# Optimization experiments

Measured on AMD Instinct MI355X. Metric: run time of the kernel, lower is better.

Reference implementation:

```python
import jax, jax.numpy as jnp
import numpy as np

N = 50000
E = 800000
IN_CH = 256
HID = 64
HEADS = 8
OUT_CH = 16
NEG_SLOPE = 0.2


def _glorot(key, shape):
    fan_in, fan_out = shape[0], shape[-1]
    lim = float(np.sqrt(6.0 / (fan_in + fan_out)))
    return jax.random.uniform(key, shape, jnp.float32, -lim, lim)


def setup_inputs() -> dict:
    key = jax.random.key(0)
    ks = jax.random.split(key, 12)
    x = jax.random.normal(ks[0], (N, IN_CH), jnp.float32)
    edge_index = jax.random.randint(ks[1], (2, E), 0, N, jnp.int64)
    # layer 1: GATConv(256 -> 64, heads=8)
    W1 = _glorot(ks[2], (IN_CH, HEADS * HID))
    a_src1 = _glorot(ks[3], (HEADS, HID))
    a_dst1 = _glorot(ks[4], (HEADS, HID))
    b1 = jnp.zeros((HEADS * HID,), jnp.float32)
    # layer 2: GATConv(512 -> 16, heads=1, concat=False)
    W2 = _glorot(ks[5], (HEADS * HID, OUT_CH))
    a_src2 = _glorot(ks[6], (1, OUT_CH))
    a_dst2 = _glorot(ks[7], (1, OUT_CH))
    b2 = jnp.zeros((OUT_CH,), jnp.float32)
    return {"x": x, "edge_index": edge_index, "W1": W1, "a_src1": a_src1,
            "a_dst1": a_dst1, "b1": b1, "W2": W2, "a_src2": a_src2,
            "a_dst2": a_dst2, "b2": b2}


def _gat_conv(x, src, dst, W, a_src, a_dst, bias, heads, out_ch, concat):
    n = x.shape[0]
    h = (x @ W).reshape(n, heads, out_ch)            # [N,H,C]
    alpha_s = jnp.einsum('nhc,hc->nh', h, a_src)      # [N,H]
    alpha_d = jnp.einsum('nhc,hc->nh', h, a_dst)
    e = alpha_s[src] + alpha_d[dst]                   # [E,H]
    e = jnp.where(e > 0, e, NEG_SLOPE * e)            # leaky_relu
    # segment softmax over incoming edges of each dst node
    e_max = jax.ops.segment_max(e, dst, num_segments=n)
    e_max = jnp.where(jnp.isfinite(e_max), e_max, 0.0)
    p = jnp.exp(e - e_max[dst])                       # [E,H]
    denom = jax.ops.segment_sum(p, dst, num_segments=n)
    alpha = p / (denom[dst] + 1e-16)                  # [E,H]
    msg = h[src] * alpha[:, :, None]                  # [E,H,C]
    out = jax.ops.segment_sum(msg, dst, num_segments=n)  # [N,H,C]
    if concat:
        out = out.reshape(n, heads * out_ch)
    else:
        out = out.mean(axis=1)
    return out + bias


def reference(x, edge_index, W1, a_src1, a_dst1, b1, W2, a_src2, a_dst2, b2):
    n = x.shape[0]
    loops = jnp.arange(n, dtype=edge_index.dtype)
    ei = jnp.concatenate([edge_index, jnp.stack([loops, loops])], axis=1)
    src, dst = ei[0], ei[1]
    h = _gat_conv(x, src, dst, W1, a_src1, a_dst1, b1, HEADS, HID, True)
    h = jax.nn.elu(h)
    out = _gat_conv(h, src, dst, W2, a_src2, a_dst2, b2, 1, OUT_CH, False)
    return jax.nn.log_softmax(out, axis=-1)
```

## Files before the change

kernel.cpp:

```cpp
#include <hip/hip_runtime.h>
#include <math.h>

#define IN_CH 256
#define HID 64
#define HEADS 8
#define F1 512
#define OUT_CH 16
#define NEG 0.2f

typedef __attribute__((ext_vector_type(8))) short bf16x8;
typedef __attribute__((ext_vector_type(4))) float f32x4;
typedef __attribute__((ext_vector_type(2))) float f32x2;

__device__ __forceinline__ unsigned short f2bf(float f) {
  unsigned int u = __builtin_bit_cast(unsigned int, f);
  u += 0x7FFFu + ((u >> 16) & 1u);
  return (unsigned short)(u >> 16);
}
__device__ __forceinline__ void gld_lds16(const void* g, void* l) {
  __builtin_amdgcn_global_load_lds(
      (const __attribute__((address_space(1))) unsigned int*)g,
      (__attribute__((address_space(3))) unsigned int*)l, 16, 0, 0);
}


__global__ void prep_kernel(const int* __restrict__ ei, int E, int N,
                            int* counts,
                            const float* __restrict__ W1, unsigned short* __restrict__ W1R,
                            const float* __restrict__ W2, unsigned short* __restrict__ W2T) {
  int idx = blockIdx.x * blockDim.x + threadIdx.x;
  int ET = E + N;
  if (idx < ET) {
    int dst = (idx < E) ? ei[E + idx] : (idx - E);
    atomicAdd(&counts[dst], 1);
  }
  if (idx < F1 * IN_CH) {
    int n = idx >> 8, k = idx & 255;
    int r = (((k >> 5) * 4 + ((k >> 3) & 3)) * 512 + n) * 8 + (k & 7);
    W1R[r] = f2bf(W1[k * F1 + n]);
  }
  if (idx < OUT_CH * F1) {
    int n = idx >> 9, k = idx & 511;
    W2T[idx] = f2bf(W2[k * OUT_CH + n]);
  }
}

__global__ __launch_bounds__(1024) void scan1_kernel(const int* __restrict__ counts,
                                                     int* __restrict__ offsets,
                                                     int* __restrict__ bsum, int n) {
  __shared__ int lds[1024];
  int t = threadIdx.x;
  int i = blockIdx.x * 1024 + t;
  int v = (i < n) ? counts[i] : 0;
  lds[t] = v;
  __syncthreads();
  for (int off = 1; off < 1024; off <<= 1) {
    int u = (t >= off) ? lds[t - off] : 0;
    __syncthreads();
    lds[t] += u;
    __syncthreads();
  }
  if (i < n) offsets[i] = lds[t] - v;
  if (t == 1023) bsum[blockIdx.x] = lds[1023];
}

__global__ __launch_bounds__(1024) void scan3b_kernel(int* __restrict__ offsets,
                                                      const int* __restrict__ bsum,
                                                      int nb, int n) {
  __shared__ int s_pre, s_tot;
  int t = threadIdx.x;
  if (t < 64) {
    int v = (t < nb) ? bsum[t] : 0;
    int vp = (t < (int)blockIdx.x) ? v : 0;
    #pragma unroll
    for (int off = 1; off < 64; off <<= 1) {
      vp += __shfl_xor(vp, off);
      v  += __shfl_xor(v, off);
    }
    if (t == 0) { s_pre = vp; s_tot = v; }
  }
  __syncthreads();
  int i = blockIdx.x * 1024 + t;
  if (i < n) offsets[i] += s_pre;
  if (blockIdx.x == 0 && t == 0) offsets[n] = s_tot;
}

__global__ void fill_kernel(const int* __restrict__ ei, int E, int N,
                            const int* __restrict__ offsets, int* cursor,
                            int* __restrict__ csr_src) {
  int e = blockIdx.x * blockDim.x + threadIdx.x;
  int ET = E + N;
  if (e >= ET) return;
  int src, dst;
  if (e < E) { src = ei[e]; dst = ei[E + e]; }
  else       { src = e - E; dst = e - E; }
  int pos = atomicAdd(&cursor[dst], 1);
  csr_src[offsets[dst] + pos] = src;
}


__global__ __launch_bounds__(512) void gemm1_mfma(const float* __restrict__ X,
                                                  const unsigned short* __restrict__ W1R,
                                                  const float* __restrict__ Asrc,
                                                  const float* __restrict__ Adst,
                                                  unsigned char* __restrict__ C,
                                                  float2* __restrict__ aad1, int M) {
  __shared__ __align__(16) short sB[4 * 512 * 8];
  int tid = threadIdx.x, w = tid >> 6, l = tid & 63;
  int wm = (w >> 2) * 32;
  int wn = (w & 3) * 128;
  int bm = blockIdx.x * 64;
  f32x4 acc[2][8];
  #pragma unroll
  for (int mi = 0; mi < 2; ++mi)
    #pragma unroll
    for (int nj = 0; nj < 8; ++nj) acc[mi][nj] = (f32x4){0.f, 0.f, 0.f, 0.f};
  int kslot = l >> 4;
  for (int kb = 0; kb < 8; ++kb) {
    __syncthreads();
    const unsigned short* src = W1R + kb * 16384;
    #pragma unroll
    for (int i = 0; i < 4; ++i)
      gld_lds16(src + (size_t)(i * 512 + tid) * 8, (char*)sB + (i * 512 + tid) * 16);
    bf16x8 af[2];
    int kbase = kb * 32 + kslot * 8;
    #pragma unroll
    for (int mi = 0; mi < 2; ++mi) {
      int r = bm + wm + mi * 16 + (l & 15);
      if (r >= M) r = M - 1;
      const float* ap = X + (size_t)r * IN_CH + kbase;
      float4 a0 = *(const float4*)ap;
      float4 a1 = *(const float4*)(ap + 4);
      unsigned int u0, u1, u2, u3;
      asm("v_cvt_pk_bf16_f32 %0, %1, %2" : "=v"(u0) : "v"(a0.x), "v"(a0.y));
      asm("v_cvt_pk_bf16_f32 %0, %1, %2" : "=v"(u1) : "v"(a0.z), "v"(a0.w));
      asm("v_cvt_pk_bf16_f32 %0, %1, %2" : "=v"(u2) : "v"(a1.x), "v"(a1.y));
      asm("v_cvt_pk_bf16_f32 %0, %1, %2" : "=v"(u3) : "v"(a1.z), "v"(a1.w));
      int4 pk = make_int4(u0, u1, u2, u3);
      af[mi] = __builtin_bit_cast(bf16x8, pk);
    }
    __syncthreads();
    #pragma unroll
    for (int nj = 0; nj < 8; ++nj) {
      int n = wn + nj * 16 + (l & 15);
      bf16x8 bf = *(const bf16x8*)&sB[(kslot * 512 + n) * 8];
      acc[0][nj] = __builtin_amdgcn_mfma_f32_16x16x32_bf16(af[0], bf, acc[0][nj], 0, 0, 0);
      acc[1][nj] = __builtin_amdgcn_mfma_f32_16x16x32_bf16(af[1], bf, acc[1][nj], 0, 0, 0);
    }
  }
  float asv[8], adv[8];
  #pragma unroll
  for (int nj = 0; nj < 8; ++nj) {
    int c = wn + nj * 16 + (l & 15);
    asv[nj] = Asrc[c]; adv[nj] = Adst[c];
  }
  int h0 = (w & 3) * 2;
  #pragma unroll
  for (int mi = 0; mi < 2; ++mi) {
    #pragma unroll
    for (int j = 0; j < 4; ++j) {
      int r = bm + wm + mi * 16 + (l >> 4) * 4 + j;
      bool ok = (r < M);
      if (ok) {
        #pragma unroll
        for (int njp = 0; njp < 4; ++njp) {
          int u = __builtin_amdgcn_cvt_pk_fp8_f32(acc[mi][2 * njp][j],
                                                  acc[mi][2 * njp + 1][j], 0, false);
          int c0 = wn + (2 * njp) * 16 + (l & 15);
          C[(size_t)r * F1 + c0]      = (unsigned char)u;
          C[(size_t)r * F1 + c0 + 16] = (unsigned char)(u >> 8);
        }
      }
      float sA = 0.f, dA = 0.f, sB2 = 0.f, dB2 = 0.f;
      #pragma unroll
      for (int nj = 0; nj < 4; ++nj) {
        float v = acc[mi][nj][j];
        sA += v * asv[nj]; dA += v * adv[nj];
      }
      #pragma unroll
      for (int nj = 4; nj < 8; ++nj) {
        float v = acc[mi][nj][j];
        sB2 += v * asv[nj]; dB2 += v * adv[nj];
      }
      #pragma unroll
      for (int off = 1; off < 16; off <<= 1) {
        sA += __shfl_xor(sA, off); dA += __shfl_xor(dA, off);
        sB2 += __shfl_xor(sB2, off); dB2 += __shfl_xor(dB2, off);
      }
      if (ok && (l & 15) == 0) {
        aad1[r * HEADS + h0]     = make_float2(sA, dA);
        aad1[r * HEADS + h0 + 1] = make_float2(sB2, dB2);
      }
    }
  }
}


__global__ __launch_bounds__(256) void aggr1_kernel(const uint2* __restrict__ h1q,
                                                    const float2* __restrict__ aad1,
                                                    const int* __restrict__ offsets,
                                                    const int* __restrict__ csr_src,
                                                    const float* __restrict__ b1,
                                                    uint4* __restrict__ out1v, int N) {
  int tid = threadIdx.x;
  int w = tid >> 6, l = tid & 63;
  int b = blockIdx.x;
  int nwg = gridDim.x;
  int q = nwg >> 3, r = nwg & 7;
  int xcd = b & 7, bi = b >> 3;
  int swz = (xcd < r) ? (xcd * (q + 1) + bi) : (r * (q + 1) + (xcd - r) * q + bi);
  int node = swz * 4 + w;
  if (node >= N) return;
  int beg = offsets[node], deg = offsets[node + 1] - beg;
  int he = l & 7;
  int hc = l >> 3;
  float adv = aad1[node * HEADS + he].y;
  float pden = 0.f;
  f32x2 acc2[4];
  #pragma unroll
  for (int i = 0; i < 4; ++i) acc2[i] = (f32x2){0.f, 0.f};
  int e = l >> 3;
  for (int c0 = 0; c0 < deg; c0 += 8) {
    int cnt = min(8, deg - c0);
    int s8 = 0;
    float p8 = 0.f;
    if (e < cnt) {
      s8 = csr_src[beg + c0 + e];
      float2 sd = aad1[s8 * HEADS + he];
      float ev = sd.x + adv;
      ev = (ev > 0.f) ? ev : NEG * ev;
      p8 = __expf(ev);
      pden += p8;
    }
    if (cnt == 8) {
      int ss[8]; float qq[8];
      #pragma unroll
      for (int j = 0; j < 8; ++j) {
        ss[j] = __shfl(s8, j * 8);
        qq[j] = __shfl(p8, j * 8 + hc);
      }
      uint2 v[8];
      #pragma unroll
      for (int j = 0; j < 8; ++j) v[j] = h1q[(size_t)ss[j] * 64 + l];
      #pragma unroll
      for (int j = 0; j < 8; ++j) {
        f32x2 p2 = (f32x2){qq[j], qq[j]};
        acc2[0] += p2 * __builtin_amdgcn_cvt_pk_f32_fp8(v[j].x, false);
        acc2[1] += p2 * __builtin_amdgcn_cvt_pk_f32_fp8(v[j].x, true);
        acc2[2] += p2 * __builtin_amdgcn_cvt_pk_f32_fp8(v[j].y, false);
        acc2[3] += p2 * __builtin_amdgcn_cvt_pk_f32_fp8(v[j].y, true);
      }
    } else {
      for (int j = 0; j < cnt; ++j) {
        int s = __shfl(s8, j * 8);
        float p = __shfl(p8, j * 8 + hc);
        uint2 v = h1q[(size_t)s * 64 + l];
        f32x2 p2 = (f32x2){p, p};
        acc2[0] += p2 * __builtin_amdgcn_cvt_pk_f32_fp8(v.x, false);
        acc2[1] += p2 * __builtin_amdgcn_cvt_pk_f32_fp8(v.x, true);
        acc2[2] += p2 * __builtin_amdgcn_cvt_pk_f32_fp8(v.y, false);
        acc2[3] += p2 * __builtin_amdgcn_cvt_pk_f32_fp8(v.y, true);
      }
    }
  }
  pden += __shfl_xor(pden, 8);
  pden += __shfl_xor(pden, 16);
  pden += __shfl_xor(pden, 32);
  float den = __shfl(pden, hc) + 1e-16f;
  float4 bv0 = *(const float4*)&b1[l * 8];
  float4 bv1 = *(const float4*)&b1[l * 8 + 4];
  float o[8];
  o[0] = acc2[0][0] / den + bv0.x; o[1] = acc2[0][1] / den + bv0.y;
  o[2] = acc2[1][0] / den + bv0.z; o[3] = acc2[1][1] / den + bv0.w;
  o[4] = acc2[2][0] / den + bv1.x; o[5] = acc2[2][1] / den + bv1.y;
  o[6] = acc2[3][0] / den + bv1.z; o[7] = acc2[3][1] / den + bv1.w;
  #pragma unroll
  for (int i = 0; i < 8; ++i) o[i] = (o[i] > 0.f) ? o[i] : expm1f(o[i]);
  uint4 ov;
  ov.x = (unsigned int)f2bf(o[0]) | ((unsigned int)f2bf(o[1]) << 16);
  ov.y = (unsigned int)f2bf(o[2]) | ((unsigned int)f2bf(o[3]) << 16);
  ov.z = (unsigned int)f2bf(o[4]) | ((unsigned int)f2bf(o[5]) << 16);
  ov.w = (unsigned int)f2bf(o[6]) | ((unsigned int)f2bf(o[7]) << 16);
  out1v[(size_t)node * 64 + l] = ov;
}


__global__ __launch_bounds__(256) void gemm2_mfma(const unsigned short* __restrict__ A,
                                                  const unsigned short* __restrict__ W2T,
                                                  const float* __restrict__ a_src2,
                                                  const float* __restrict__ a_dst2,
                                                  float* __restrict__ t2,
                                                  float2* __restrict__ aad2, int M) {
  __shared__ __align__(16) short sW[16 * 512];
  int tid = threadIdx.x, w = tid >> 6, l = tid & 63;
  for (int i = tid; i < 1024; i += 256) ((uint4*)sW)[i] = ((const uint4*)W2T)[i];
  __syncthreads();
  int bm = blockIdx.x * 128 + w * 32;
  f32x4 acc[2];
  acc[0] = (f32x4){0.f, 0.f, 0.f, 0.f};
  acc[1] = (f32x4){0.f, 0.f, 0.f, 0.f};
  int rl = l & 15;
  int koff = (l >> 4) * 8;
  int r0 = bm + rl;       if (r0 >= M) r0 = M - 1;
  int r1 = bm + 16 + rl;  if (r1 >= M) r1 = M - 1;
  const unsigned short* a0p = A + (size_t)r0 * F1 + koff;
  const unsigned short* a1p = A + (size_t)r1 * F1 + koff;
  #pragma unroll
  for (int k0 = 0; k0 < F1; k0 += 32) {
    bf16x8 bfv = *(const bf16x8*)&sW[rl * 512 + k0 + koff];
    bf16x8 af0 = *(const bf16x8*)(a0p + k0);
    bf16x8 af1 = *(const bf16x8*)(a1p + k0);
    acc[0] = __builtin_amdgcn_mfma_f32_16x16x32_bf16(af0, bfv, acc[0], 0, 0, 0);
    acc[1] = __builtin_amdgcn_mfma_f32_16x16x32_bf16(af1, bfv, acc[1], 0, 0, 0);
  }
  float asv = a_src2[rl], adv = a_dst2[rl];
  #pragma unroll
  for (int mi = 0; mi < 2; ++mi) {
    #pragma unroll
    for (int j = 0; j < 4; ++j) {
      int r = bm + mi * 16 + (l >> 4) * 4 + j;
      float val = acc[mi][j];
      float s = val * asv, d = val * adv;
      s += __shfl_xor(s, 1); s += __shfl_xor(s, 2); s += __shfl_xor(s, 4); s += __shfl_xor(s, 8);
      d += __shfl_xor(d, 1); d += __shfl_xor(d, 2); d += __shfl_xor(d, 4); d += __shfl_xor(d, 8);
      if (r < M) {
        t2[(size_t)r * OUT_CH + rl] = val;
        if (rl == 0) aad2[r] = make_float2(s, d);
      }
    }
  }
}


__global__ __launch_bounds__(256) void aggr2_kernel(const float* __restrict__ t2,
                                                    const float2* __restrict__ aad2,
                                                    const int* __restrict__ offsets,
                                                    const int* __restrict__ csr_src,
                                                    const float* __restrict__ b2,
                                                    float* __restrict__ out, int N) {
  int tid = threadIdx.x;
  int node = blockIdx.x * 4 + (tid >> 6);
  int lane = tid & 63;
  if (node >= N) return;
  int beg = offsets[node];
  int deg = offsets[node + 1] - beg;
  float ad = aad2[node].y;
  float acc = 0.f, den = 0.f;
  int eg = lane >> 4, c = lane & 15;
  for (int base = 0; base < deg; base += 8) {
    int j1 = base + eg;
    int j2 = base + 4 + eg;
    bool ok1 = j1 < deg, ok2 = j2 < deg;
    int s1 = csr_src[beg + (ok1 ? j1 : 0)];
    int s2 = csr_src[beg + (ok2 ? j2 : 0)];
    float2 m1 = aad2[s1];
    float2 m2 = aad2[s2];
    float t1v = t2[(size_t)s1 * OUT_CH + c];
    float t2v = t2[(size_t)s2 * OUT_CH + c];
    float e1 = m1.x + ad;
    e1 = (e1 > 0.f) ? e1 : NEG * e1;
    float p1 = ok1 ? __expf(e1) : 0.f;
    float e2 = m2.x + ad;
    e2 = (e2 > 0.f) ? e2 : NEG * e2;
    float p2 = ok2 ? __expf(e2) : 0.f;
    acc += p1 * t1v + p2 * t2v;
    if (c == 0) den += p1 + p2;
  }
  acc += __shfl_xor(acc, 16); acc += __shfl_xor(acc, 32);
  den += __shfl_xor(den, 16); den += __shfl_xor(den, 32);
  den = __shfl(den, 0);
  float val = acc / (den + 1e-16f) + b2[c];
  float mx = val;
  #pragma unroll
  for (int off = 1; off < 16; off <<= 1) mx = fmaxf(mx, __shfl_xor(mx, off));
  float ex = __expf(val - mx);
  float se = ex;
  #pragma unroll
  for (int off = 1; off < 16; off <<= 1) se += __shfl_xor(se, off);
  float ls = val - mx - logf(se);
  if (lane < 16) out[(size_t)node * OUT_CH + lane] = ls;
}


extern "C" void kernel_launch(void* const* d_in, const int* in_sizes, int n_in,
                              void* d_out, int out_size, void* d_ws, size_t ws_size,
                              hipStream_t stream) {
  const float* x      = (const float*)d_in[0];
  const int*   ei     = (const int*)d_in[1];
  const float* W1     = (const float*)d_in[2];
  const float* a_src1 = (const float*)d_in[3];
  const float* a_dst1 = (const float*)d_in[4];
  const float* b1     = (const float*)d_in[5];
  const float* W2     = (const float*)d_in[6];
  const float* a_src2 = (const float*)d_in[7];
  const float* a_dst2 = (const float*)d_in[8];
  const float* b2     = (const float*)d_in[9];
  float* out = (float*)d_out;

  int N = in_sizes[0] / IN_CH;
  int E = in_sizes[1] / 2;
  int ET = E + N;

  char* w = (char*)d_ws;
  auto alloc = [&](size_t bytes) -> void* {
    void* p = (void*)w;
    w += (bytes + 255) & ~(size_t)255;
    return p;
  };
  unsigned char*  h1b   = (unsigned char*)alloc((size_t)N * F1);
  unsigned short* out1b = (unsigned short*)alloc((size_t)N * F1 * 2);
  unsigned short* w1r   = (unsigned short*)alloc((size_t)F1 * IN_CH * 2);
  unsigned short* w2t   = (unsigned short*)alloc((size_t)OUT_CH * F1 * 2);
  float* aad1  = (float*)alloc((size_t)N * HEADS * 8);
  float* t2    = (float*)alloc((size_t)N * OUT_CH * 4);
  float* aad2  = (float*)alloc((size_t)N * 8);
  int* counts  = (int*)alloc((size_t)N * 2 * 4);
  int* cursor  = counts + N;
  int* offsets = (int*)alloc((size_t)(N + 1) * 4);
  int* bsum    = (int*)alloc(256 * 4);
  int* csr_src = (int*)alloc((size_t)ET * 4);

  int nb = (N + 1023) / 1024;

  hipMemsetAsync(counts, 0, (size_t)N * 2 * 4, stream);
  prep_kernel<<<(ET + 255) / 256, 256, 0, stream>>>(ei, E, N, counts, W1, w1r, W2, w2t);
  scan1_kernel<<<nb, 1024, 0, stream>>>(counts, offsets, bsum, N);
  scan3b_kernel<<<nb, 1024, 0, stream>>>(offsets, bsum, nb, N);
  fill_kernel<<<(ET + 255) / 256, 256, 0, stream>>>(ei, E, N, offsets, cursor, csr_src);

  gemm1_mfma<<<(N + 63) / 64, 512, 0, stream>>>(x, w1r, a_src1, a_dst1, h1b,
                                                (float2*)aad1, N);
  aggr1_kernel<<<(N + 3) / 4, 256, 0, stream>>>((const uint2*)h1b, (const float2*)aad1,
                                                offsets, csr_src, b1, (uint4*)out1b, N);
  gemm2_mfma<<<(N + 127) / 128, 256, 0, stream>>>(out1b, w2t, a_src2, a_dst2, t2,
                                                  (float2*)aad2, N);
  aggr2_kernel<<<(N + 3) / 4, 256, 0, stream>>>(t2, (const float2*)aad2, offsets, csr_src,
                                                b2, out, N);
}
```

Baseline: 259.7 us.

## Fuse layer-2 GEMM into aggregation epilogue and merge scan kernels via grid barrier

The layer-1 aggregation now keeps each block's four ELU-activated bf16 rows in shared memory, and one wavefront runs a 16x16x32 MFMA against W2T to produce t2 and the layer-2 attention logits directly. This drops the out1b intermediate (N×512 bf16 written then re-read) and the separate gemm2 launch. The two-pass prefix scan becomes a single kernel that uses an atomic spin barrier across blocks, which assumes all scan blocks are resident at the same time. The fused epilogue wastes MFMA rows, since only 4 of 16 are valid, and serialises it on one wave per block, adding tail time to the aggregation kernel.

New measurement: 271.5 us. 1.05x slower.

```diff
diff --git a/kernel.cpp b/kernel.cpp
--- a/kernel.cpp
+++ b/kernel.cpp
@@ -45,10 +45,14 @@
   }
 }
 
-__global__ __launch_bounds__(1024) void scan1_kernel(const int* __restrict__ counts,
-                                                     int* __restrict__ offsets,
-                                                     int* __restrict__ bsum, int n) {
+
+__global__ __launch_bounds__(1024) void scan_kernel(const int* __restrict__ counts,
+                                                    int* __restrict__ offsets,
+                                                    int* __restrict__ bsum,
+                                                    int* bars, int n) {
   __shared__ int lds[1024];
+  __shared__ int s_pre, s_tot;
+  int nb = gridDim.x;
   int t = threadIdx.x;
   int i = blockIdx.x * 1024 + t;
   int v = (i < n) ? counts[i] : 0;
@@ -60,28 +64,27 @@
     lds[t] += u;
     __syncthreads();
   }
-  if (i < n) offsets[i] = lds[t] - v;
-  if (t == 1023) bsum[blockIdx.x] = lds[1023];
-}
-
-__global__ __launch_bounds__(1024) void scan3b_kernel(int* __restrict__ offsets,
-                                                      const int* __restrict__ bsum,
-                                                      int nb, int n) {
-  __shared__ int s_pre, s_tot;
-  int t = threadIdx.x;
+  int incl = lds[t];
+  if (t == 1023) bsum[blockIdx.x] = incl;
+  __syncthreads();
+  if (t == 0) {
+    __threadfence();
+    atomicAdd(&bars[0], 1);
+    while (atomicAdd(&bars[0], 0) < nb) __builtin_amdgcn_s_sleep(8);
+  }
+  __syncthreads();
   if (t < 64) {
-    int v = (t < nb) ? bsum[t] : 0;
-    int vp = (t < (int)blockIdx.x) ? v : 0;
+    int bv = (t < nb) ? bsum[t] : 0;
+    int vp = (t < (int)blockIdx.x) ? bv : 0;
     #pragma unroll
     for (int off = 1; off < 64; off <<= 1) {
       vp += __shfl_xor(vp, off);
-      v  += __shfl_xor(v, off);
-    }
-    if (t == 0) { s_pre = vp; s_tot = v; }
+      bv += __shfl_xor(bv, off);
+    }
+    if (t == 0) { s_pre = vp; s_tot = bv; }
   }
   __syncthreads();
-  int i = blockIdx.x * 1024 + t;
-  if (i < n) offsets[i] += s_pre;
+  if (i < n) offsets[i] = s_pre + incl - v;
   if (blockIdx.x == 0 && t == 0) offsets[n] = s_tot;
 }
 
@@ -196,12 +199,17 @@
 }
 
 
-__global__ __launch_bounds__(256) void aggr1_kernel(const uint2* __restrict__ h1q,
-                                                    const float2* __restrict__ aad1,
-                                                    const int* __restrict__ offsets,
-                                                    const int* __restrict__ csr_src,
-                                                    const float* __restrict__ b1,
-                                                    uint4* __restrict__ out1v, int N) {
+__global__ __launch_bounds__(256) void aggr1_fused(const uint2* __restrict__ h1q,
+                                                   const float2* __restrict__ aad1,
+                                                   const int* __restrict__ offsets,
+                                                   const int* __restrict__ csr_src,
+                                                   const float* __restrict__ b1,
+                                                   const unsigned short* __restrict__ W2T,
+                                                   const float* __restrict__ a_src2,
+                                                   const float* __restrict__ a_dst2,
+                                                   float* __restrict__ t2,
+                                                   float2* __restrict__ aad2, int N) {
+  __shared__ __align__(16) unsigned short s_h[4][512];
   int tid = threadIdx.x;
   int w = tid >> 6, l = tid & 63;
   int b = blockIdx.x;
@@ -209,123 +217,106 @@
   int q = nwg >> 3, r = nwg & 7;
   int xcd = b & 7, bi = b >> 3;
   int swz = (xcd < r) ? (xcd * (q + 1) + bi) : (r * (q + 1) + (xcd - r) * q + bi);
-  int node = swz * 4 + w;
-  if (node >= N) return;
-  int beg = offsets[node], deg = offsets[node + 1] - beg;
-  int he = l & 7;
-  int hc = l >> 3;
-  float adv = aad1[node * HEADS + he].y;
-  float pden = 0.f;
-  f32x2 acc2[4];
-  #pragma unroll
-  for (int i = 0; i < 4; ++i) acc2[i] = (f32x2){0.f, 0.f};
-  int e = l >> 3;
-  for (int c0 = 0; c0 < deg; c0 += 8) {
-    int cnt = min(8, deg - c0);
-    int s8 = 0;
-    float p8 = 0.f;
-    if (e < cnt) {
-      s8 = csr_src[beg + c0 + e];
-      float2 sd = aad1[s8 * HEADS + he];
-      float ev = sd.x + adv;
-      ev = (ev > 0.f) ? ev : NEG * ev;
-      p8 = __expf(ev);
-      pden += p8;
-    }
-    if (cnt == 8) {
-      int ss[8]; float qq[8];
-      #pragma unroll
-      for (int j = 0; j < 8; ++j) {
-        ss[j] = __shfl(s8, j * 8);
-        qq[j] = __shfl(p8, j * 8 + hc);
-      }
-      uint2 v[8];
-      #pragma unroll
-      for (int j = 0; j < 8; ++j) v[j] = h1q[(size_t)ss[j] * 64 + l];
-      #pragma unroll
-      for (int j = 0; j < 8; ++j) {
-        f32x2 p2 = (f32x2){qq[j], qq[j]};
-        acc2[0] += p2 * __builtin_amdgcn_cvt_pk_f32_fp8(v[j].x, false);
-        acc2[1] += p2 * __builtin_amdgcn_cvt_pk_f32_fp8(v[j].x, true);
-        acc2[2] += p2 * __builtin_amdgcn_cvt_pk_f32_fp8(v[j].y, false);
-        acc2[3] += p2 * __builtin_amdgcn_cvt_pk_f32_fp8(v[j].y, true);
-      }
-    } else {
-      for (int j = 0; j < cnt; ++j) {
-        int s = __shfl(s8, j * 8);
-        float p = __shfl(p8, j * 8 + hc);
-        uint2 v = h1q[(size_t)s * 64 + l];
-        f32x2 p2 = (f32x2){p, p};
-        acc2[0] += p2 * __builtin_amdgcn_cvt_pk_f32_fp8(v.x, false);
-        acc2[1] += p2 * __builtin_amdgcn_cvt_pk_f32_fp8(v.x, true);
-        acc2[2] += p2 * __builtin_amdgcn_cvt_pk_f32_fp8(v.y, false);
-        acc2[3] += p2 * __builtin_amdgcn_cvt_pk_f32_fp8(v.y, true);
-      }
-    }
-  }
-  pden += __shfl_xor(pden, 8);
-  pden += __shfl_xor(pden, 16);
-  pden += __shfl_xor(pden, 32);
-  float den = __shfl(pden, hc) + 1e-16f;
-  float4 bv0 = *(const float4*)&b1[l * 8];
-  float4 bv1 = *(const float4*)&b1[l * 8 + 4];
-  float o[8];
-  o[0] = acc2[0][0] / den + bv0.x; o[1] = acc2[0][1] / den + bv0.y;
-  o[2] = acc2[1][0] / den + bv0.z; o[3] = acc2[1][1] / den + bv0.w;
-  o[4] = acc2[2][0] / den + bv1.x; o[5] = acc2[2][1] / den + bv1.y;
-  o[6] = acc2[3][0] / den + bv1.z; o[7] = acc2[3][1] / den + bv1.w;
-  #pragma unroll
-  for (int i = 0; i < 8; ++i) o[i] = (o[i] > 0.f) ? o[i] : expm1f(o[i]);
-  uint4 ov;
-  ov.x = (unsigned int)f2bf(o[0]) | ((unsigned int)f2bf(o[1]) << 16);
-  ov.y = (unsigned int)f2bf(o[2]) | ((unsigned int)f2bf(o[3]) << 16);
-  ov.z = (unsigned int)f2bf(o[4]) | ((unsigned int)f2bf(o[5]) << 16);
-  ov.w = (unsigned int)f2bf(o[6]) | ((unsigned int)f2bf(o[7]) << 16);
-  out1v[(size_t)node * 64 + l] = ov;
-}
-
-
-__global__ __launch_bounds__(256) void gemm2_mfma(const unsigned short* __restrict__ A,
-                                                  const unsigned short* __restrict__ W2T,
-                                                  const float* __restrict__ a_src2,
-                                                  const float* __restrict__ a_dst2,
-                                                  float* __restrict__ t2,
-                                                  float2* __restrict__ aad2, int M) {
-  __shared__ __align__(16) short sW[16 * 512];
-  int tid = threadIdx.x, w = tid >> 6, l = tid & 63;
-  for (int i = tid; i < 1024; i += 256) ((uint4*)sW)[i] = ((const uint4*)W2T)[i];
+  int nodeBase = swz * 4;
+  int node = nodeBase + w;
+  bool active = node < N;
+  if (active) {
+    int beg = offsets[node], deg = offsets[node + 1] - beg;
+    int he = l & 7;
+    int hc = l >> 3;
+    float adv = aad1[node * HEADS + he].y;
+    float pden = 0.f;
+    f32x2 acc2[4];
+    #pragma unroll
+    for (int i = 0; i < 4; ++i) acc2[i] = (f32x2){0.f, 0.f};
+    int e = l >> 3;
+    for (int c0 = 0; c0 < deg; c0 += 8) {
+      int cnt = min(8, deg - c0);
+      int s8 = 0;
+      float p8 = 0.f;
+      if (e < cnt) {
+        s8 = csr_src[beg + c0 + e];
+        float2 sd = aad1[s8 * HEADS + he];
+        float ev = sd.x + adv;
+        ev = (ev > 0.f) ? ev : NEG * ev;
+        p8 = __expf(ev);
+        pden += p8;
+      }
+      if (cnt == 8) {
+        int ss[8]; float qq[8];
+        #pragma unroll
+        for (int j = 0; j < 8; ++j) {
+          ss[j] = __shfl(s8, j * 8);
+          qq[j] = __shfl(p8, j * 8 + hc);
+        }
+        uint2 v[8];
+        #pragma unroll
+        for (int j = 0; j < 8; ++j) v[j] = h1q[(size_t)ss[j] * 64 + l];
+        #pragma unroll
+        for (int j = 0; j < 8; ++j) {
+          f32x2 p2 = (f32x2){qq[j], qq[j]};
+          acc2[0] += p2 * __builtin_amdgcn_cvt_pk_f32_fp8(v[j].x, false);
+          acc2[1] += p2 * __builtin_amdgcn_cvt_pk_f32_fp8(v[j].x, true);
+          acc2[2] += p2 * __builtin_amdgcn_cvt_pk_f32_fp8(v[j].y, false);
+          acc2[3] += p2 * __builtin_amdgcn_cvt_pk_f32_fp8(v[j].y, true);
+        }
+      } else {
+        for (int j = 0; j < cnt; ++j) {
+          int s = __shfl(s8, j * 8);
+          float p = __shfl(p8, j * 8 + hc);
+          uint2 v = h1q[(size_t)s * 64 + l];
+          f32x2 p2 = (f32x2){p, p};
+          acc2[0] += p2 * __builtin_amdgcn_cvt_pk_f32_fp8(v.x, false);
+          acc2[1] += p2 * __builtin_amdgcn_cvt_pk_f32_fp8(v.x, true);
+          acc2[2] += p2 * __builtin_amdgcn_cvt_pk_f32_fp8(v.y, false);
+          acc2[3] += p2 * __builtin_amdgcn_cvt_pk_f32_fp8(v.y, true);
+        }
+      }
+    }
+    pden += __shfl_xor(pden, 8);
+    pden += __shfl_xor(pden, 16);
+    pden += __shfl_xor(pden, 32);
+    float den = __shfl(pden, hc) + 1e-16f;
+    float4 bv0 = *(const float4*)&b1[l * 8];
+    float4 bv1 = *(const float4*)&b1[l * 8 + 4];
+    float o[8];
+    o[0] = acc2[0][0] / den + bv0.x; o[1] = acc2[0][1] / den + bv0.y;
+    o[2] = acc2[1][0] / den + bv0.z; o[3] = acc2[1][1] / den + bv0.w;
+    o[4] = acc2[2][0] / den + bv1.x; o[5] = acc2[2][1] / den + bv1.y;
+    o[6] = acc2[3][0] / den + bv1.z; o[7] = acc2[3][1] / den + bv1.w;
+    #pragma unroll
+    for (int i = 0; i < 8; ++i) o[i] = (o[i] > 0.f) ? o[i] : expm1f(o[i]);
+    uint4 ov;
+    ov.x = (unsigned int)f2bf(o[0]) | ((unsigned int)f2bf(o[1]) << 16);
+    ov.y = (unsigned int)f2bf(o[2]) | ((unsigned int)f2bf(o[3]) << 16);
+    ov.z = (unsigned int)f2bf(o[4]) | ((unsigned int)f2bf(o[5]) << 16);
+    ov.w = (unsigned int)f2bf(o[6]) | ((unsigned int)f2bf(o[7]) << 16);
+    *(uint4*)&s_h[w][l * 8] = ov;
+  }
   __syncthreads();
-  int bm = blockIdx.x * 128 + w * 32;
-  f32x4 acc[2];
-  acc[0] = (f32x4){0.f, 0.f, 0.f, 0.f};
-  acc[1] = (f32x4){0.f, 0.f, 0.f, 0.f};
-  int rl = l & 15;
-  int koff = (l >> 4) * 8;
-  int r0 = bm + rl;       if (r0 >= M) r0 = M - 1;
-  int r1 = bm + 16 + rl;  if (r1 >= M) r1 = M - 1;
-  const unsigned short* a0p = A + (size_t)r0 * F1 + koff;
-  const unsigned short* a1p = A + (size_t)r1 * F1 + koff;
-  #pragma unroll
-  for (int k0 = 0; k0 < F1; k0 += 32) {
-    bf16x8 bfv = *(const bf16x8*)&sW[rl * 512 + k0 + koff];
-    bf16x8 af0 = *(const bf16x8*)(a0p + k0);
-    bf16x8 af1 = *(const bf16x8*)(a1p + k0);
-    acc[0] = __builtin_amdgcn_mfma_f32_16x16x32_bf16(af0, bfv, acc[0], 0, 0, 0);
-    acc[1] = __builtin_amdgcn_mfma_f32_16x16x32_bf16(af1, bfv, acc[1], 0, 0, 0);
-  }
-  float asv = a_src2[rl], adv = a_dst2[rl];
-  #pragma unroll
-  for (int mi = 0; mi < 2; ++mi) {
+  if (w == 0) {
+    f32x4 acc = (f32x4){0.f, 0.f, 0.f, 0.f};
+    int col = l & 15;
+    int ks = (l >> 4) * 8;
+    int rl = l & 3;
+    #pragma unroll
+    for (int k0 = 0; k0 < F1; k0 += 32) {
+      bf16x8 af = *(const bf16x8*)&s_h[rl][k0 + ks];
+      bf16x8 bf = *(const bf16x8*)&W2T[col * 512 + k0 + ks];
+      acc = __builtin_amdgcn_mfma_f32_16x16x32_bf16(af, bf, acc, 0, 0, 0);
+    }
+    float a2sv = a_src2[col], a2dv = a_dst2[col];
+    bool rowsValid = ((l >> 4) == 0);
     #pragma unroll
     for (int j = 0; j < 4; ++j) {
-      int r = bm + mi * 16 + (l >> 4) * 4 + j;
-      float val = acc[mi][j];
-      float s = val * asv, d = val * adv;
+      float val = acc[j];
+      float s = val * a2sv, d = val * a2dv;
       s += __shfl_xor(s, 1); s += __shfl_xor(s, 2); s += __shfl_xor(s, 4); s += __shfl_xor(s, 8);
       d += __shfl_xor(d, 1); d += __shfl_xor(d, 2); d += __shfl_xor(d, 4); d += __shfl_xor(d, 8);
-      if (r < M) {
-        t2[(size_t)r * OUT_CH + rl] = val;
-        if (rl == 0) aad2[r] = make_float2(s, d);
+      int nd = nodeBase + j;
+      if (rowsValid && nd < N) {
+        t2[(size_t)nd * OUT_CH + col] = val;
+        if (col == 0) aad2[nd] = make_float2(s, d);
       }
     }
   }
@@ -408,32 +399,30 @@
     return p;
   };
   unsigned char*  h1b   = (unsigned char*)alloc((size_t)N * F1);
-  unsigned short* out1b = (unsigned short*)alloc((size_t)N * F1 * 2);
   unsigned short* w1r   = (unsigned short*)alloc((size_t)F1 * IN_CH * 2);
   unsigned short* w2t   = (unsigned short*)alloc((size_t)OUT_CH * F1 * 2);
   float* aad1  = (float*)alloc((size_t)N * HEADS * 8);
   float* t2    = (float*)alloc((size_t)N * OUT_CH * 4);
   float* aad2  = (float*)alloc((size_t)N * 8);
-  int* counts  = (int*)alloc((size_t)N * 2 * 4);
+  int* counts  = (int*)alloc((size_t)N * 2 * 4 + 256);
   int* cursor  = counts + N;
+  int* bars    = counts + 2 * N;
   int* offsets = (int*)alloc((size_t)(N + 1) * 4);
   int* bsum    = (int*)alloc(256 * 4);
   int* csr_src = (int*)alloc((size_t)ET * 4);
 
   int nb = (N + 1023) / 1024;
 
-  hipMemsetAsync(counts, 0, (size_t)N * 2 * 4, stream);
+  hipMemsetAsync(counts, 0, (size_t)N * 2 * 4 + 256, stream);
   prep_kernel<<<(ET + 255) / 256, 256, 0, stream>>>(ei, E, N, counts, W1, w1r, W2, w2t);
-  scan1_kernel<<<nb, 1024, 0, stream>>>(counts, offsets, bsum, N);
-  scan3b_kernel<<<nb, 1024, 0, stream>>>(offsets, bsum, nb, N);
+  scan_kernel<<<nb, 1024, 0, stream>>>(counts, offsets, bsum, bars, N);
   fill_kernel<<<(ET + 255) / 256, 256, 0, stream>>>(ei, E, N, offsets, cursor, csr_src);
 
   gemm1_mfma<<<(N + 63) / 64, 512, 0, stream>>>(x, w1r, a_src1, a_dst1, h1b,
                                                 (float2*)aad1, N);
-  aggr1_kernel<<<(N + 3) / 4, 256, 0, stream>>>((const uint2*)h1b, (const float2*)aad1,
-                                                offsets, csr_src, b1, (uint4*)out1b, N);
-  gemm2_mfma<<<(N + 127) / 128, 256, 0, stream>>>(out1b, w2t, a_src2, a_dst2, t2,
-                                                  (float2*)aad2, N);
+  aggr1_fused<<<(N + 3) / 4, 256, 0, stream>>>((const uint2*)h1b, (const float2*)aad1,
+                                               offsets, csr_src, b1, w2t, a_src2, a_dst2,
+                                               t2, (float2*)aad2, N);
   aggr2_kernel<<<(N + 3) / 4, 256, 0, stream>>>(t2, (const float2*)aad2, offsets, csr_src,
                                                 b2, out, N);
 }
```
